# Kernel tuning notes

Hardware: AMD Instinct MI355X
Metric: run time of the kernel (lower is better)

The kernel has to match this reference:

```python
import jax, jax.numpy as jnp
import numpy as np

N, H = 131072, 256          # rows, hidden_dim
P, K_OCC, K_SUBJ = 16, 8, 16  # phases, occurrences per phase, subjects per occurrence
O = P * K_OCC               # 128 total occurrence classes
S = O * K_SUBJ              # 2048 total subject classes


def setup_inputs() -> dict:
    key = jax.random.key(0)
    ks = jax.random.split(key, 10)
    X = jax.random.normal(ks[0], (N, H), jnp.float32)
    X_phase = jax.random.randint(ks[1], (N,), 0, P)
    X_occ_local = jax.random.randint(ks[2], (N,), 0, K_OCC)
    X_subj_local = jax.random.randint(ks[3], (N,), 0, K_SUBJ)
    sc = 1.0 / np.sqrt(H)  # nn.Linear default init range
    W_phase = jax.random.uniform(ks[4], (P, H), jnp.float32, -sc, sc)
    b_phase = jax.random.uniform(ks[5], (P,), jnp.float32, -sc, sc)
    W_p2o = jax.random.uniform(ks[6], (O, H), jnp.float32, -sc, sc)      # stacked phase_to_occurrence Linears
    b_p2o = jax.random.uniform(ks[7], (O,), jnp.float32, -sc, sc)
    W_o2s = jax.random.uniform(ks[8], (S, H), jnp.float32, -sc, sc)      # stacked occurrence_to_subj Linears
    b_o2s = jax.random.uniform(ks[9], (S,), jnp.float32, -sc, sc)
    return {
        "X": X, "W_phase": W_phase, "b_phase": b_phase,
        "W_p2o": W_p2o, "b_p2o": b_p2o, "W_o2s": W_o2s, "b_o2s": b_o2s,
        "X_phase": X_phase, "X_occ_local": X_occ_local, "X_subj_local": X_subj_local,
    }


def reference(X, W_phase, b_phase, W_p2o, b_p2o, W_o2s, b_o2s,
              X_phase, X_occ_local, X_subj_local):
    n = X.shape[0]
    rows = jnp.arange(n)

    # phase head: softmax over all P phases, pick the true phase prob
    phase_proba = jax.nn.softmax(X @ W_phase.T + b_phase, axis=1)[rows, X_phase]  # [N]

    # occurrence head: per-sample small Linear chosen by phase key -> compute all
    # stacked logits once, gather the phase's K_OCC-block, softmax within block
    occ_logits = (X @ W_p2o.T + b_p2o).reshape(n, P, K_OCC)[rows, X_phase]        # [N, K_OCC]
    occ_proba = jax.nn.softmax(occ_logits, axis=1)[rows, X_occ_local]             # [N]

    # subject head: same pattern keyed by global occurrence id
    X_occurrence = X_phase * K_OCC + X_occ_local                                   # global occ ids
    subj_logits = (X @ W_o2s.T + b_o2s).reshape(n, O, K_SUBJ)[rows, X_occurrence]  # [N, K_SUBJ]
    subj_proba = jax.nn.softmax(subj_logits, axis=1)[rows, X_subj_local]           # [N]

    po = phase_proba * occ_proba
    return (phase_proba, po, po * subj_proba)
```

## Files before the change

kernel.cpp:

```cpp
#include <hip/hip_runtime.h>

#define H_ 256
#define P_ 16
#define KOCC 8
#define KSUBJ 16
#define O_ 128
#define CAPMAX 2048

typedef __attribute__((ext_vector_type(8))) __bf16 bf16x8;
typedef __attribute__((ext_vector_type(4))) float f32x4;

__device__ __forceinline__ bf16x8 load_bf8(const float* p) {
  float4 a = *(const float4*)p;
  float4 b = *(const float4*)(p + 4);
  bf16x8 r;
  r[0] = (__bf16)a.x; r[1] = (__bf16)a.y; r[2] = (__bf16)a.z; r[3] = (__bf16)a.w;
  r[4] = (__bf16)b.x; r[5] = (__bf16)b.y; r[6] = (__bf16)b.z; r[7] = (__bf16)b.w;
  return r;
}

__device__ __forceinline__ bf16x8 cvt_bf8(float4 a, float4 b) {
  bf16x8 r;
  r[0] = (__bf16)a.x; r[1] = (__bf16)a.y; r[2] = (__bf16)a.z; r[3] = (__bf16)a.w;
  r[4] = (__bf16)b.x; r[5] = (__bf16)b.y; r[6] = (__bf16)b.z; r[7] = (__bf16)b.w;
  return r;
}

__device__ __forceinline__ float rsum16(float v) {
  v += __shfl_xor(v, 1);
  v += __shfl_xor(v, 2);
  v += __shfl_xor(v, 4);
  v += __shfl_xor(v, 8);
  return v;
}

__global__ __launch_bounds__(1024) void scatter_kernel(
    const int* __restrict__ xp, const int* __restrict__ xo,
    int* counts, int* brows, int n, int cap) {
  __shared__ int hist[O_];
  __shared__ int basev[O_];
  int tid = threadIdx.x;
  if (tid < O_) hist[tid] = 0;
  __syncthreads();
  int base_i = blockIdx.x * 4096 + tid;
  int be[4], pos[4];
#pragma unroll
  for (int e = 0; e < 4; ++e) {
    int i = base_i + e * 1024;
    pos[e] = -1;
    if (i < n) {
      be[e] = xp[i] * KOCC + xo[i];
      pos[e] = atomicAdd(&hist[be[e]], 1);
    }
  }
  __syncthreads();
  if (tid < O_) basev[tid] = atomicAdd(&counts[tid], hist[tid]);
  __syncthreads();
#pragma unroll
  for (int e = 0; e < 4; ++e) {
    if (pos[e] >= 0) {
      int idx = basev[be[e]] + pos[e];
      if (idx < cap) brows[be[e] * cap + idx] = base_i + e * 1024;
    }
  }
}

__device__ __forceinline__ void issue_group(
    const int* __restrict__ brow_b, const int* __restrict__ subj,
    const float* __restrict__ X, int base, int count, int col, int quad,
    int& rida, int& subjv, int& rem, float4* ta, float4* tb) {
  rem = count - base;
  rida = brow_b[base + (col < rem ? col : rem - 1)];
  subjv = subj[rida];
  const float* xr = X + (size_t)rida * H_ + quad * 8;
#pragma unroll
  for (int kk = 0; kk < 8; ++kk) {
    const float4* s = (const float4*)(xr + kk * 32);
    ta[kk] = s[0];
    tb[kk] = s[1];
  }
}

__device__ __forceinline__ void process_group(
    const bf16x8* __restrict__ Bfrag, int lane, int col, int quad,
    int p, int occl, bool v1, float bias0, float bias1, float bias2,
    int rida, int subjv, int rem, const float4* ta, const float4* tb,
    float* __restrict__ out, int n) {
  f32x4 acc0 = {0.f, 0.f, 0.f, 0.f};
  f32x4 acc1 = {0.f, 0.f, 0.f, 0.f};
  f32x4 acc2 = {0.f, 0.f, 0.f, 0.f};
#pragma unroll
  for (int kk = 0; kk < 8; ++kk) {
    bf16x8 a = cvt_bf8(ta[kk], tb[kk]);
    acc0 = __builtin_amdgcn_mfma_f32_16x16x32_bf16(a, Bfrag[kk * 64 + lane], acc0, 0, 0, 0);
    acc1 = __builtin_amdgcn_mfma_f32_16x16x32_bf16(a, Bfrag[(8 + kk) * 64 + lane], acc1, 0, 0, 0);
    acc2 = __builtin_amdgcn_mfma_f32_16x16x32_bf16(a, Bfrag[(16 + kk) * 64 + lane], acc2, 0, 0, 0);
  }
#pragma unroll
  for (int r = 0; r < 4; ++r) {
    int rloc = quad * 4 + r;
    bool rv = rloc < rem;
    int ridr = __shfl(rida, rloc);
    int tsub = __shfl(subjv, rloc);
    float e0 = __expf(acc0[r] + bias0);
    float s0 = rsum16(e0);
    float p0 = __shfl(e0, quad * 16 + p) / s0;
    float e1 = v1 ? __expf(acc1[r] + bias1) : 0.0f;
    float s1 = rsum16(e1);
    float p1 = __shfl(e1, quad * 16 + occl) / s1;
    float e2 = __expf(acc2[r] + bias2);
    float s2 = rsum16(e2);
    float p2 = __shfl(e2, quad * 16 + tsub) / s2;
    if (col == 0 && rv) {
      float po = p0 * p1;
      out[ridr] = p0;
      out[n + ridr] = po;
      out[2 * n + ridr] = po * p2;
    }
  }
}

__global__ __launch_bounds__(256, 2) void hsm_main(
    const float* __restrict__ X,
    const float* __restrict__ Wp, const float* __restrict__ bp,
    const float* __restrict__ Wo, const float* __restrict__ bo,
    const float* __restrict__ Ws, const float* __restrict__ bs,
    const int* __restrict__ subj,
    const int* __restrict__ counts, const int* __restrict__ brows,
    float* __restrict__ out, int n, int cap) {
  int b = blockIdx.x & 127;
  int chunk = blockIdx.x >> 7;
  int count = counts[b];
  if (count > cap) count = cap;
  int p = b >> 3;
  int occl = b & 7;

  __shared__ __bf16 Bf[3 * 8 * 64 * 8];
  {
    int t = threadIdx.x;
#pragma unroll
    for (int it = 0; it < 6; ++it) {
      int fid = it * 256 + t;
      int lane_f = fid & 63;
      int hk = fid >> 6;
      int head = hk >> 3, kk = hk & 7;
      int colf = lane_f & 15, quadf = lane_f >> 4;
      const float* src;
      if (head == 0)      src = Wp + colf * H_;
      else if (head == 1) src = Wo + (p * KOCC + (colf & 7)) * H_;
      else                src = Ws + (b * KSUBJ + colf) * H_;
      bf16x8 v = load_bf8(src + kk * 32 + quadf * 8);
      *(bf16x8*)&Bf[(size_t)fid * 8] = v;
    }
  }
  __syncthreads();

  int lane = threadIdx.x & 63;
  int wave = threadIdx.x >> 6;
  int col = lane & 15;
  int quad = lane >> 4;

  bool v1 = col < KOCC;
  float bias0 = bp[col];
  float bias1 = v1 ? bo[p * KOCC + col] : 0.0f;
  float bias2 = bs[b * KSUBJ + col];

  const int* brow_b = brows + b * cap;
  const bf16x8* Bfrag = (const bf16x8*)Bf;

  int base = chunk * 64 + wave * 16;
  if (base >= count) return;

  float4 taA[8], tbA[8], taB[8], tbB[8];
  int ridaA, subjA, remA, ridaB, subjB, remB;
  issue_group(brow_b, subj, X, base, count, col, quad, ridaA, subjA, remA, taA, tbA);
  while (true) {
    bool vB = (base + 256) < count;
    if (vB)
      issue_group(brow_b, subj, X, base + 256, count, col, quad, ridaB, subjB, remB, taB, tbB);
    __builtin_amdgcn_sched_barrier(0);
    process_group(Bfrag, lane, col, quad, p, occl, v1, bias0, bias1, bias2,
                  ridaA, subjA, remA, taA, tbA, out, n);
    if (!vB) break;
    bool vA2 = (base + 512) < count;
    if (vA2)
      issue_group(brow_b, subj, X, base + 512, count, col, quad, ridaA, subjA, remA, taA, tbA);
    __builtin_amdgcn_sched_barrier(0);
    process_group(Bfrag, lane, col, quad, p, occl, v1, bias0, bias1, bias2,
                  ridaB, subjB, remB, taB, tbB, out, n);
    if (!vA2) break;
    base += 512;
  }
}

extern "C" void kernel_launch(void* const* d_in, const int* in_sizes, int n_in,
                              void* d_out, int out_size, void* d_ws, size_t ws_size,
                              hipStream_t stream) {
  const float* X  = (const float*)d_in[0];
  const float* Wp = (const float*)d_in[1];
  const float* bp = (const float*)d_in[2];
  const float* Wo = (const float*)d_in[3];
  const float* bo = (const float*)d_in[4];
  const float* Ws = (const float*)d_in[5];
  const float* bs = (const float*)d_in[6];
  const int* xp   = (const int*)d_in[7];
  const int* xo   = (const int*)d_in[8];
  const int* xs   = (const int*)d_in[9];
  float* out = (float*)d_out;
  int n = in_sizes[7];

  int* wsI = (int*)d_ws;
  int* counts = wsI;
  int* brows = wsI + 128;
  long avail = (long)(ws_size / 4) - 128;
  int cap = (int)(avail / O_);
  if (cap > CAPMAX) cap = CAPMAX;
  if (cap < 1) cap = 1;

  hipMemsetAsync(counts, 0, O_ * sizeof(int), stream);
  scatter_kernel<<<dim3((n + 4095) / 4096), dim3(1024), 0, stream>>>(xp, xo, counts, brows, n, cap);
  hsm_main<<<dim3(O_ * 4), dim3(256), 0, stream>>>(X, Wp, bp, Wo, bo, Ws, bs, xs,
                                                   counts, brows, out, n, cap);
}
```

Baseline: 222.0 us.

## Pack subject id with row index in scatter and prefetch bucket rows upfront

The scatter kernel now packs each row index together with its subject label into one int, so the main kernel no longer does a dependent gather of the subject array. The main kernel loads every bucket row index for the wave up front into registers, which removes the dependent index load from the X-prefetch chain. Scatter blocks now handle 1024 rows each instead of 4096, and the softmax divides become hardware reciprocal multiplies. Packing assumes n < 2^20 and the cap limits each wave to at most 8 groups; the reciprocal is slightly less accurate than a true divide.

```diff
diff --git a/kernel.cpp b/kernel.cpp
--- a/kernel.cpp
+++ b/kernel.cpp
@@ -6,6 +6,7 @@
 #define KSUBJ 16
 #define O_ 128
 #define CAPMAX 2048
+#define RMASK 0xFFFFF
 
 typedef __attribute__((ext_vector_type(8))) __bf16 bf16x8;
 typedef __attribute__((ext_vector_type(4))) float f32x4;
@@ -36,42 +37,31 @@
 
 __global__ __launch_bounds__(1024) void scatter_kernel(
     const int* __restrict__ xp, const int* __restrict__ xo,
+    const int* __restrict__ xs,
     int* counts, int* brows, int n, int cap) {
   __shared__ int hist[O_];
   __shared__ int basev[O_];
   int tid = threadIdx.x;
   if (tid < O_) hist[tid] = 0;
   __syncthreads();
-  int base_i = blockIdx.x * 4096 + tid;
-  int be[4], pos[4];
-#pragma unroll
-  for (int e = 0; e < 4; ++e) {
-    int i = base_i + e * 1024;
-    pos[e] = -1;
-    if (i < n) {
-      be[e] = xp[i] * KOCC + xo[i];
-      pos[e] = atomicAdd(&hist[be[e]], 1);
-    }
+  int i = blockIdx.x * 1024 + tid;
+  int be = 0, pos = -1, pack = 0;
+  if (i < n) {
+    be = xp[i] * KOCC + xo[i];
+    pack = i | (xs[i] << 20);
+    pos = atomicAdd(&hist[be], 1);
   }
   __syncthreads();
   if (tid < O_) basev[tid] = atomicAdd(&counts[tid], hist[tid]);
   __syncthreads();
-#pragma unroll
-  for (int e = 0; e < 4; ++e) {
-    if (pos[e] >= 0) {
-      int idx = basev[be[e]] + pos[e];
-      if (idx < cap) brows[be[e] * cap + idx] = base_i + e * 1024;
-    }
-  }
-}
-
-__device__ __forceinline__ void issue_group(
-    const int* __restrict__ brow_b, const int* __restrict__ subj,
-    const float* __restrict__ X, int base, int count, int col, int quad,
-    int& rida, int& subjv, int& rem, float4* ta, float4* tb) {
-  rem = count - base;
-  rida = brow_b[base + (col < rem ? col : rem - 1)];
-  subjv = subj[rida];
+  if (pos >= 0) {
+    int idx = basev[be] + pos;
+    if (idx < cap) brows[be * cap + idx] = pack;
+  }
+}
+
+__device__ __forceinline__ void issue_x(
+    const float* __restrict__ X, int rida, int quad, float4* ta, float4* tb) {
   const float* xr = X + (size_t)rida * H_ + quad * 8;
 #pragma unroll
   for (int kk = 0; kk < 8; ++kk) {
@@ -84,7 +74,7 @@
 __device__ __forceinline__ void process_group(
     const bf16x8* __restrict__ Bfrag, int lane, int col, int quad,
     int p, int occl, bool v1, float bias0, float bias1, float bias2,
-    int rida, int subjv, int rem, const float4* ta, const float4* tb,
+    int pkv, int rem, const float4* ta, const float4* tb,
     float* __restrict__ out, int n) {
   f32x4 acc0 = {0.f, 0.f, 0.f, 0.f};
   f32x4 acc1 = {0.f, 0.f, 0.f, 0.f};
@@ -100,17 +90,18 @@
   for (int r = 0; r < 4; ++r) {
     int rloc = quad * 4 + r;
     bool rv = rloc < rem;
-    int ridr = __shfl(rida, rloc);
-    int tsub = __shfl(subjv, rloc);
+    int pkr = __shfl(pkv, rloc);
+    int ridr = pkr & RMASK;
+    int tsub = pkr >> 20;
     float e0 = __expf(acc0[r] + bias0);
     float s0 = rsum16(e0);
-    float p0 = __shfl(e0, quad * 16 + p) / s0;
+    float p0 = __shfl(e0, quad * 16 + p) * __builtin_amdgcn_rcpf(s0);
     float e1 = v1 ? __expf(acc1[r] + bias1) : 0.0f;
     float s1 = rsum16(e1);
-    float p1 = __shfl(e1, quad * 16 + occl) / s1;
+    float p1 = __shfl(e1, quad * 16 + occl) * __builtin_amdgcn_rcpf(s1);
     float e2 = __expf(acc2[r] + bias2);
     float s2 = rsum16(e2);
-    float p2 = __shfl(e2, quad * 16 + tsub) / s2;
+    float p2 = __shfl(e2, quad * 16 + tsub) * __builtin_amdgcn_rcpf(s2);
     if (col == 0 && rv) {
       float po = p0 * p1;
       out[ridr] = p0;
@@ -125,7 +116,6 @@
     const float* __restrict__ Wp, const float* __restrict__ bp,
     const float* __restrict__ Wo, const float* __restrict__ bo,
     const float* __restrict__ Ws, const float* __restrict__ bs,
-    const int* __restrict__ subj,
     const int* __restrict__ counts, const int* __restrict__ brows,
     float* __restrict__ out, int n, int cap) {
   int b = blockIdx.x & 127;
@@ -170,26 +160,31 @@
 
   int base = chunk * 64 + wave * 16;
   if (base >= count) return;
+  int ng = (count - base + 255) >> 8;
+
+  int pk[8];
+#pragma unroll
+  for (int j = 0; j < 8; ++j) {
+    pk[j] = 0;
+    if (j < ng) {
+      int bj = base + (j << 8);
+      int rem = count - bj;
+      pk[j] = brow_b[bj + (col < rem ? col : rem - 1)];
+    }
+  }
 
   float4 taA[8], tbA[8], taB[8], tbB[8];
-  int ridaA, subjA, remA, ridaB, subjB, remB;
-  issue_group(brow_b, subj, X, base, count, col, quad, ridaA, subjA, remA, taA, tbA);
-  while (true) {
-    bool vB = (base + 256) < count;
-    if (vB)
-      issue_group(brow_b, subj, X, base + 256, count, col, quad, ridaB, subjB, remB, taB, tbB);
+  issue_x(X, pk[0] & RMASK, quad, taA, tbA);
+#pragma unroll
+  for (int j = 0; j < 8; ++j) {
+    if (j >= ng) break;
+    if (j + 1 < ng)
+      issue_x(X, pk[(j + 1) & 7] & RMASK, quad,
+              (j & 1) ? taA : taB, (j & 1) ? tbA : tbB);
     __builtin_amdgcn_sched_barrier(0);
     process_group(Bfrag, lane, col, quad, p, occl, v1, bias0, bias1, bias2,
-                  ridaA, subjA, remA, taA, tbA, out, n);
-    if (!vB) break;
-    bool vA2 = (base + 512) < count;
-    if (vA2)
-      issue_group(brow_b, subj, X, base + 512, count, col, quad, ridaA, subjA, remA, taA, tbA);
-    __builtin_amdgcn_sched_barrier(0);
-    process_group(Bfrag, lane, col, quad, p, occl, v1, bias0, bias1, bias2,
-                  ridaB, subjB, remB, taB, tbB, out, n);
-    if (!vA2) break;
-    base += 512;
+                  pk[j], count - (base + (j << 8)),
+                  (j & 1) ? taB : taA, (j & 1) ? tbB : tbA, out, n);
   }
 }
 
@@ -218,7 +213,8 @@
   if (cap < 1) cap = 1;
 
   hipMemsetAsync(counts, 0, O_ * sizeof(int), stream);
-  scatter_kernel<<<dim3((n + 4095) / 4096), dim3(1024), 0, stream>>>(xp, xo, counts, brows, n, cap);
-  hsm_main<<<dim3(O_ * 4), dim3(256), 0, stream>>>(X, Wp, bp, Wo, bo, Ws, bs, xs,
+  scatter_kernel<<<dim3((n + 1023) / 1024), dim3(1024), 0, stream>>>(
+      xp, xo, xs, counts, brows, n, cap);
+  hsm_main<<<dim3(O_ * 4), dim3(256), 0, stream>>>(X, Wp, bp, Wo, bo, Ws, bs,
                                                    counts, brows, out, n, cap);
 }
```

New measurement: 223.6 us. Within noise of the previous version (+0.7%).
